# Optimization experiments

Measured on AMD Instinct MI355X. Metric: run time of the kernel, lower is better.

Reference implementation:

```python
import jax, jax.numpy as jnp
import numpy as np

D_MODEL = 2048
NQ = 16      # query heads
NKV = 4      # kv heads (GQA)
DH = 128     # content head dim
DR = 64      # rope head dim
DKV = 512    # kv latent dim
DQC = 1536   # q latent dim
B, S = 2, 2048
DT = DH + DR


def rotate_half(x):
    x1, x2 = jnp.split(x, 2, axis=-1)
    return jnp.concatenate([-x2, x1], axis=-1)


def setup_inputs() -> dict:
    key = jax.random.key(0)
    ks = jax.random.split(key, 10)
    sc = 0.02
    x = jax.random.normal(ks[0], (B, S, D_MODEL), jnp.float32)
    positions = jnp.arange(S, dtype=jnp.int32)
    # standard RoPE cache over the rope subspace
    inv_freq = 1.0 / (10000.0 ** (jnp.arange(0, DR, 2, dtype=jnp.float32) / DR))
    ang = positions.astype(jnp.float32)[:, None] * inv_freq[None, :]   # [S, DR/2]
    emb = jnp.concatenate([ang, ang], axis=-1)                         # [S, DR]
    cos_cache = jnp.cos(emb)
    sin_cache = jnp.sin(emb)
    attn_mask = jnp.tril(jnp.ones((S, S), dtype=bool))                 # causal, True=attend
    # weights stored [in, out] (torch Linear weight transposed)
    W_DKV = sc * jax.random.normal(ks[1], (D_MODEL, DKV), jnp.float32)
    W_UK = sc * jax.random.normal(ks[2], (DKV, NKV * DH), jnp.float32)
    W_UV = sc * jax.random.normal(ks[3], (DKV, NKV * DH), jnp.float32)
    W_DQ = sc * jax.random.normal(ks[4], (D_MODEL, DQC), jnp.float32)
    W_UQ = sc * jax.random.normal(ks[5], (DQC, NQ * DH), jnp.float32)
    W_KR = sc * jax.random.normal(ks[6], (D_MODEL, NKV * DR), jnp.float32)
    W_QR = sc * jax.random.normal(ks[7], (D_MODEL, NQ * DR), jnp.float32)
    W_O = sc * jax.random.normal(ks[8], (NQ * DH, D_MODEL), jnp.float32)
    return {"x": x, "cos_cache": cos_cache, "sin_cache": sin_cache,
            "positions": positions, "attn_mask": attn_mask,
            "W_DKV": W_DKV, "W_UK": W_UK, "W_UV": W_UV, "W_DQ": W_DQ,
            "W_UQ": W_UQ, "W_KR": W_KR, "W_QR": W_QR, "W_O": W_O}


def reference(x, cos_cache, sin_cache, positions, attn_mask,
              W_DKV, W_UK, W_UV, W_DQ, W_UQ, W_KR, W_QR, W_O):
    b, s, _ = x.shape
    cos = cos_cache[positions][None, None]  # [1,1,S,DR]
    sin = sin_cache[positions][None, None]
    # low-rank KV latent (this is the MLA cache)
    c_kv = x @ W_DKV                                                 # [B,S,DKV]
    K_rope = (x @ W_KR).reshape(b, s, NKV, DR).transpose(0, 2, 1, 3)  # [B,NKV,S,DR]
    K_rope = K_rope * cos + rotate_half(K_rope) * sin
    # decompress K/V content from latent
    K_content = (c_kv @ W_UK).reshape(b, s, NKV, DH).transpose(0, 2, 1, 3)  # [B,NKV,S,DH]
    V = (c_kv @ W_UV).reshape(b, s, NKV, DH).transpose(0, 2, 1, 3)          # [B,NKV,S,DH]
    # queries via low-rank path + rope subspace
    c_q = x @ W_DQ
    Q_content = (c_q @ W_UQ).reshape(b, s, NQ, DH).transpose(0, 2, 1, 3)    # [B,NQ,S,DH]
    Q_rope = (x @ W_QR).reshape(b, s, NQ, DR).transpose(0, 2, 1, 3)         # [B,NQ,S,DR]
    Q_rope = Q_rope * cos + rotate_half(Q_rope) * sin
    Q = jnp.concatenate([Q_content, Q_rope], axis=-1)   # [B,NQ,S,DT]
    K = jnp.concatenate([K_content, K_rope], axis=-1)   # [B,NKV,S,DT]
    # GQA: group query heads over shared kv heads (no materialized repeat)
    G = NQ // NKV
    Qg = Q.reshape(b, NKV, G, s, DT)
    scores = jnp.einsum('bkgsd,bktd->bkgst', Qg, K) / np.float32(np.sqrt(DT))
    scores = jnp.where(attn_mask[None, None, None], scores, -jnp.inf)
    w = jax.nn.softmax(scores, axis=-1)
    attn = jnp.einsum('bkgst,bktd->bkgsd', w, V)         # [B,NKV,G,S,DH]
    attn = attn.reshape(b, NQ, s, DH).transpose(0, 2, 1, 3).reshape(b, s, NQ * DH)
    out = attn @ W_O                                     # [B,S,D_MODEL]
    return out, c_kv, K_rope
```

## Files before the change

kernel.cpp:

```cpp
#include <hip/hip_runtime.h>
#include <stdint.h>

typedef unsigned short u16;
typedef unsigned int u32;

#define B_    2
#define S_    2048
#define NQ_   16
#define NKV_  4
#define DH_   128
#define DR_   64
#define DT_   192
#define M_    4096

using short8 = __attribute__((ext_vector_type(8))) short;
using f32x4  = __attribute__((ext_vector_type(4))) float;
using half8  = __attribute__((ext_vector_type(8))) _Float16;
using u16x4  = __attribute__((ext_vector_type(4))) u16;

__device__ __forceinline__ float cl(float f) {
    return fminf(fmaxf(f, -3.38e38f), 3.38e38f);
}
__device__ __forceinline__ u16 f2b(float f) {
    union { float f; u32 u; } v; v.f = f;
    u32 u = v.u;
    return (u16)((u + 0x7fffu + ((u >> 16) & 1u)) >> 16);
}
__device__ __forceinline__ void gload16(const void* g, void* l) {
    __builtin_amdgcn_global_load_lds(
        (const __attribute__((address_space(1))) void*)g,
        (__attribute__((address_space(3))) void*)l,
        16, 0, 0);
}

__device__ __forceinline__ void wt_body(const float* __restrict__ W,
                                        _Float16* __restrict__ T,
                                        int K, int N, int kx, int ny,
                                        float (*tile)[33]) {
    int k0 = kx * 32, n0 = ny * 32;
    int tx = threadIdx.x, ty = threadIdx.y;
#pragma unroll
    for (int i = 0; i < 32; i += 8)
        tile[ty + i][tx] = W[(size_t)(k0 + ty + i) * N + n0 + tx];
    __syncthreads();
#pragma unroll
    for (int i = 0; i < 32; i += 8)
        T[(size_t)(n0 + ty + i) * K + k0 + tx] = (_Float16)tile[tx][ty + i];
}

__global__ __launch_bounds__(256) void prep_all(const float* __restrict__ x,
                                                _Float16* __restrict__ xf,
                                                const float* __restrict__ W_DKV,
                                                const float* __restrict__ W_KR,
                                                const float* __restrict__ W_DQ,
                                                const float* __restrict__ W_QR,
                                                const float* __restrict__ W_UQ,
                                                const float* __restrict__ W_UK,
                                                const float* __restrict__ W_UV,
                                                const float* __restrict__ W_O,
                                                _Float16* __restrict__ Wmeg,
                                                _Float16* __restrict__ Wuq,
                                                _Float16* __restrict__ Wukv,
                                                _Float16* __restrict__ Wo) {
    __shared__ float tile[32][33];
    const int id = blockIdx.x;
    if (id < 1024) {
        wt_body(W_DKV, Wmeg, 2048, 512, id & 63, id >> 6, tile);
    } else if (id < 1536) {
        int l = id - 1024;
        wt_body(W_KR, Wmeg + (size_t)512 * 2048, 2048, 256, l & 63, l >> 6, tile);
    } else if (id < 4608) {
        int l = id - 1536;
        wt_body(W_DQ, Wmeg + (size_t)768 * 2048, 2048, 1536, l & 63, l >> 6, tile);
    } else if (id < 6656) {
        int l = id - 4608;
        wt_body(W_QR, Wmeg + (size_t)2304 * 2048, 2048, 1024, l & 63, l >> 6, tile);
    } else if (id < 9728) {
        int l = id - 6656;
        wt_body(W_UQ, Wuq, 1536, 2048, l % 48, l / 48, tile);
    } else if (id < 9984) {
        int l = id - 9728;
        wt_body(W_UK, Wukv, 512, 512, l & 15, l >> 4, tile);
    } else if (id < 10240) {
        int l = id - 9984;
        wt_body(W_UV, Wukv + (size_t)512 * 512, 512, 512, l & 15, l >> 4, tile);
    } else if (id < 14336) {
        int l = id - 10240;
        wt_body(W_O, Wo, 2048, 2048, l & 63, l >> 6, tile);
    } else {
        int l = id - 14336;
        int t1 = threadIdx.y * 32 + threadIdx.x;
        size_t i = ((size_t)l * 256 + t1) * 8;
        float4 a = *(const float4*)(x + i);
        float4 b4 = *(const float4*)(x + i + 4);
        float va[8] = {a.x, a.y, a.z, a.w, b4.x, b4.y, b4.z, b4.w};
        half8 f;
#pragma unroll
        for (int j = 0; j < 8; ++j) f[j] = (_Float16)va[j];
        *(half8*)(xf + i) = f;
    }
}

__device__ __forceinline__ void gemm_body(const _Float16* __restrict__ A, int lda,
                                          const _Float16* __restrict__ Bt,
                                          void* p0, void* p1,
                                          float cscale, int mode,
                                          int N, int K, int bx,
                                          _Float16* lA, _Float16* lB) {
    const int t = threadIdx.x, lane = t & 63, w = t >> 6;
    const int quad = lane >> 4, l16 = lane & 15;
    const int wr = w >> 1, wc = w & 1;
    const int m0 = blockIdx.y * 128, n0 = bx * 128;
    f32x4 acc[4][4] = {};

    for (int kt = 0; kt < K; kt += 32) {
        __syncthreads();
#pragma unroll
        for (int c = 0; c < 2; ++c) {
            const int chunk = c * 256 + t;
            const int row = chunk >> 2, co = (chunk & 3) * 8;
            const int lofs = (c * 256 + w * 64) * 8;
            gload16(A + (size_t)(m0 + row) * lda + kt + co, lA + lofs);
            gload16(Bt + (size_t)(n0 + row) * K + kt + co, lB + lofs);
        }
        __syncthreads();
        half8 af[4], bf4[4];
#pragma unroll
        for (int i = 0; i < 4; ++i) {
            af[i]  = *(const half8*)&lA[(wr * 64 + i * 16 + l16) * 32 + quad * 8];
            bf4[i] = *(const half8*)&lB[(wc * 64 + i * 16 + l16) * 32 + quad * 8];
        }
#pragma unroll
        for (int i = 0; i < 4; ++i)
#pragma unroll
            for (int j = 0; j < 4; ++j)
                acc[i][j] = __builtin_amdgcn_mfma_f32_16x16x32_f16(af[i], bf4[j], acc[i][j], 0, 0, 0);
    }
#pragma unroll
    for (int i = 0; i < 4; ++i)
#pragma unroll
        for (int j = 0; j < 4; ++j) {
            const int mbase = m0 + wr * 64 + i * 16 + quad * 4;
            const int nn = n0 + wc * 64 + j * 16 + l16;
            if (mode == 3) {
                const int bb = mbase >> 11, s = mbase & 2047;
                if (nn < 512) {
                    u16* Kp = (u16*)p0;
                    const int kv = nn >> 7, d = nn & 127;
                    const size_t rb = ((size_t)((bb * 4 + kv) * 2048 + s)) * 192 + d;
#pragma unroll
                    for (int r = 0; r < 4; ++r)
                        Kp[rb + (size_t)r * 192] = f2b(acc[i][j][r]);
                } else {
                    u16* Vt = (u16*)p1;
                    const int e = nn - 512, kv = e >> 7, d = e & 127;
                    u16x4 pk;
                    pk[0] = f2b(acc[i][j][0]); pk[1] = f2b(acc[i][j][1]);
                    pk[2] = f2b(acc[i][j][2]); pk[3] = f2b(acc[i][j][3]);
                    *(u16x4*)&((u16*)Vt)[((size_t)((bb * 4 + kv) * 128 + d)) * 2048 + s] = pk;
                }
            } else {
                float* C = (float*)p0;
#pragma unroll
                for (int r = 0; r < 4; ++r)
                    C[(size_t)(mbase + r) * N + nn] = cl(acc[i][j][r]);
            }
        }
}

__global__ __launch_bounds__(256) void gemm_f16(const _Float16* __restrict__ A, int lda,
                                                const _Float16* __restrict__ Bt,
                                                void* p0, void* p1,
                                                float cscale, int mode,
                                                int N, int K) {
    __shared__ __align__(16) _Float16 lA[128 * 32];
    __shared__ __align__(16) _Float16 lB[128 * 32];
    gemm_body(A, lda, Bt, p0, p1, cscale, mode, N, K, blockIdx.x, lA, lB);
}

__global__ __launch_bounds__(512) void gemm2ph(const _Float16* __restrict__ A, int lda,
                                               const _Float16* __restrict__ Bt,
                                               void* p0, void* p1, void* p2,
                                               void* p3, void* p4,
                                               float cscale, int mode,
                                               int N, int K, int NBX) {
    __shared__ __align__(16) _Float16 lA[2][128 * 64];
    __shared__ __align__(16) _Float16 lB[2][256 * 64];
    const int t = threadIdx.x, lane = t & 63, w = t >> 6;
    const int quad = lane >> 4, l16 = lane & 15;
    const int wr = w >> 2, wc = w & 3;
    const int id = blockIdx.x;
    const int cpx = (NBX * 32) >> 3;
    const int swz = (id & 7) * cpx + (id >> 3);
    const int bx = swz % NBX, by = swz / NBX;
    const int m0 = by * 128, n0 = bx * 256;
    f32x4 acc[4][4] = {};

    auto STAGE = [&](int buf, int kt) {
#pragma unroll
        for (int q = 0; q < 2; ++q) {
            const int chunk = q * 512 + t;
            const int row = chunk >> 3, cop = chunk & 7;
            const int co = (cop ^ (row & 7)) * 8;
            gload16(A + (size_t)(m0 + row) * lda + kt + co,
                    lA[buf] + (q * 512 + w * 64) * 8);
        }
#pragma unroll
        for (int q = 0; q < 4; ++q) {
            const int chunk = q * 512 + t;
            const int row = chunk >> 3, cop = chunk & 7;
            const int co = (cop ^ (row & 7)) * 8;
            gload16(Bt + (size_t)(n0 + row) * K + kt + co,
                    lB[buf] + (q * 512 + w * 64) * 8);
        }
    };

    STAGE(0, 0);
    __syncthreads();
    int cur = 0;
    for (int kt = 0; kt < K; kt += 64) {
        if (kt + 64 < K) STAGE(cur ^ 1, kt + 64);
        const _Float16* bufA = lA[cur];
        const _Float16* bufB = lB[cur];
#pragma unroll
        for (int kc = 0; kc < 2; ++kc) {
            half8 af[4], bf[4];
#pragma unroll
            for (int i = 0; i < 4; ++i) {
                const int r = wr * 64 + i * 16 + l16;
                af[i] = *(const half8*)&bufA[(r * 8 + ((kc * 4 + quad) ^ (r & 7))) * 8];
            }
#pragma unroll
            for (int j = 0; j < 4; ++j) {
                const int r = wc * 64 + j * 16 + l16;
                bf[j] = *(const half8*)&bufB[(r * 8 + ((kc * 4 + quad) ^ (r & 7))) * 8];
            }
#pragma unroll
            for (int i = 0; i < 4; ++i)
#pragma unroll
                for (int j = 0; j < 4; ++j)
                    acc[i][j] = __builtin_amdgcn_mfma_f32_16x16x32_f16(af[i], bf[j], acc[i][j], 0, 0, 0);
        }
        __syncthreads();
        cur ^= 1;
    }
#pragma unroll
    for (int i = 0; i < 4; ++i)
#pragma unroll
        for (int j = 0; j < 4; ++j) {
            const int mbase = m0 + wr * 64 + i * 16 + quad * 4;
            const int nn = n0 + wc * 64 + j * 16 + l16;
            if (mode == 0) {
                float* C = (float*)p0;
#pragma unroll
                for (int r = 0; r < 4; ++r)
                    C[(size_t)(mbase + r) * N + nn] = cl(acc[i][j][r]);
            } else if (mode == 2) {
                u16* Q = (u16*)p0;
                const int h = nn >> 7, dcol = nn & 127;
#pragma unroll
                for (int r = 0; r < 4; ++r)
                    Q[(size_t)(mbase + r) * 3072 + h * 192 + dcol] =
                        f2b(acc[i][j][r] * cscale);
            } else {
                if (nn < 512) {
                    float* ckv = (float*)p0;
                    _Float16* ckf = (_Float16*)p1;
#pragma unroll
                    for (int r = 0; r < 4; ++r) {
                        float v = acc[i][j][r];
                        ckv[(size_t)(mbase + r) * 512 + nn] = cl(v);
                        ckf[(size_t)(mbase + r) * 512 + nn] = (_Float16)v;
                    }
                } else if (nn < 768) {
                    float* krr = (float*)p2;
#pragma unroll
                    for (int r = 0; r < 4; ++r)
                        krr[(size_t)(mbase + r) * 256 + (nn - 512)] = acc[i][j][r];
                } else if (nn < 2304) {
                    _Float16* dqc = (_Float16*)p3;
#pragma unroll
                    for (int r = 0; r < 4; ++r)
                        dqc[(size_t)(mbase + r) * 1536 + (nn - 768)] = (_Float16)acc[i][j][r];
                } else {
                    _Float16* qrf = (_Float16*)p4;
#pragma unroll
                    for (int r = 0; r < 4; ++r)
                        qrf[(size_t)(mbase + r) * 1024 + (nn - 2304)] = (_Float16)acc[i][j][r];
                }
            }
        }
}

__global__ __launch_bounds__(256) void rope_all(const _Float16* __restrict__ qrf,
                                                const float* __restrict__ krr,
                                                const float* __restrict__ cosc,
                                                const float* __restrict__ sinc,
                                                const int* __restrict__ pos,
                                                u16* __restrict__ qb16,
                                                float* __restrict__ Krope,
                                                u16* __restrict__ Kp) {
    const float sc = 0.07216878364870322f;
    if ((int)blockIdx.x < 8192) {
        int t = blockIdx.x * 256 + threadIdx.x;
        int d = t & 31, h = (t >> 5) & 15, rowi = t >> 9;
        int s = rowi & 2047;
        int p = pos[s];
        float c1 = cosc[p * 64 + d],      s1 = sinc[p * 64 + d];
        float c2 = cosc[p * 64 + 32 + d], s2 = sinc[p * 64 + 32 + d];
        const _Float16* base = qrf + (size_t)rowi * 1024 + h * 64;
        float x1 = (float)base[d];
        float x2 = (float)base[d + 32];
        u16* q = qb16 + (size_t)rowi * 3072 + h * 192 + 128;
        q[d]      = f2b((x1 * c1 - x2 * s1) * sc);
        q[d + 32] = f2b((x2 * c2 + x1 * s2) * sc);
    } else {
        int t = (blockIdx.x - 8192) * 256 + threadIdx.x;
        int d = t & 31, kv = (t >> 5) & 3, rowi = t >> 7;
        int b = rowi >> 11, s = rowi & 2047;
        int p = pos[s];
        float c1 = cosc[p * 64 + d],      s1 = sinc[p * 64 + d];
        float c2 = cosc[p * 64 + 32 + d], s2 = sinc[p * 64 + 32 + d];
        float x1 = krr[(size_t)rowi * 256 + kv * 64 + d];
        float x2 = krr[(size_t)rowi * 256 + kv * 64 + 32 + d];
        float o1 = x1 * c1 - x2 * s1;
        float o2 = x2 * c2 + x1 * s2;
        int g = b * NKV_ + kv;
        size_t ob = ((size_t)(g * S_) + s) * 64;
        Krope[ob + d]      = cl(o1);
        Krope[ob + 32 + d] = cl(o2);
        u16* kp = Kp + ((size_t)(g * S_ + s)) * 192 + 128;
        kp[d]      = f2b(o1);
        kp[32 + d] = f2b(o2);
    }
}

__global__ __launch_bounds__(256) void attn_mfma(const u16* __restrict__ qb16,
                                                 const u16* __restrict__ Kp,
                                                 const u16* __restrict__ Vt,
                                                 _Float16* __restrict__ atf) {
    __shared__ __align__(16) u16 lK[64 * 200];
    __shared__ __align__(16) u16 lVt[144 * 72];
    __shared__ __align__(16) u16 lP[4][16 * 72];

    const int t = threadIdx.x, lane = t & 63, w = t >> 6;
    const int quad = lane >> 4, l16 = lane & 15;
    const int id = blockIdx.x;
    const int g = id & 7;
    const int b = g >> 2;
    const int k = id >> 3;
    const int h = (g & 3) * 4 + (k & 3);
    const int px = k >> 2;

#pragma unroll
    for (int c = 0; c < 4; ++c) {
        int i = c * 256 + t;
        int rr = 128 + (i >> 6), ccol = i & 63;
        lVt[rr * 72 + ccol] = (rr == 128) ? (u16)0x3F80 : (u16)0;
    }

    for (int ph = 0; ph < 2; ++ph) {
        const int qt = ph ? px : (31 - px);
        const int q0 = qt * 64;
        const int iw = q0 + w * 16;

        short8 qf[6];
        {
            const u16* qp = qb16 + ((size_t)(b * S_ + iw + l16)) * 3072 + h * 192;
#pragma unroll
            for (int kc = 0; kc < 6; ++kc)
                qf[kc] = *(const short8*)&qp[kc * 32 + quad * 8];
        }

        f32x4 O9[9] = {};
        float mr[4] = {-1e30f, -1e30f, -1e30f, -1e30f};

        const int ntile = qt + 1;
        for (int tile = 0; tile < ntile; ++tile) {
            const int j0 = tile * 64;
            __syncthreads();
#pragma unroll
            for (int c = 0; c < 6; ++c) {
                int seg = c * 256 + t;
                int row = seg / 24, ch = (seg % 24) * 8;
                *(uint4*)&lK[row * 200 + ch] =
                    *(const uint4*)&Kp[((size_t)g * S_ + j0 + row) * 192 + ch];
            }
#pragma unroll
            for (int c = 0; c < 4; ++c) {
                int seg = c * 256 + t;
                int d = seg >> 3, ch = (seg & 7) * 8;
                *(uint4*)&lVt[d * 72 + ch] =
                    *(const uint4*)&Vt[((size_t)g * 128 + d) * S_ + j0 + ch];
            }
            __syncthreads();

            f32x4 s4[4];
            __builtin_amdgcn_s_setprio(1);
#pragma unroll
            for (int cc = 0; cc < 4; ++cc) {
                f32x4 sx = {};
#pragma unroll
                for (int kc = 0; kc < 6; ++kc) {
                    short8 kf = *(const short8*)&lK[(cc * 16 + l16) * 200 + kc * 32 + quad * 8];
                    sx = __builtin_amdgcn_mfma_f32_16x16x32_bf16(qf[kc], kf, sx, 0, 0, 0);
                }
                s4[cc] = sx;
            }
            __builtin_amdgcn_s_setprio(0);

            float sv[4][4];
#pragma unroll
            for (int cc = 0; cc < 4; ++cc)
#pragma unroll
                for (int r = 0; r < 4; ++r) {
                    int ir = iw + quad * 4 + r;
                    sv[cc][r] = (j0 + cc * 16 + l16 <= ir) ? s4[cc][r] : -1e30f;
                }
            float tm[4];
#pragma unroll
            for (int r = 0; r < 4; ++r)
                tm[r] = fmaxf(fmaxf(sv[0][r], sv[1][r]), fmaxf(sv[2][r], sv[3][r]));
#pragma unroll
            for (int m = 1; m < 16; m <<= 1)
#pragma unroll
                for (int r = 0; r < 4; ++r) tm[r] = fmaxf(tm[r], __shfl_xor(tm[r], m));
            int small = (tm[0] <= mr[0] + 8.f) && (tm[1] <= mr[1] + 8.f) &&
                        (tm[2] <= mr[2] + 8.f) && (tm[3] <= mr[3] + 8.f);
            if (!__all(small)) {
                float al[4];
#pragma unroll
                for (int r = 0; r < 4; ++r) {
                    float mn = fmaxf(mr[r], tm[r]);
                    al[r] = __expf(mr[r] - mn);
                    mr[r] = mn;
                }
#pragma unroll
                for (int dc = 0; dc < 9; ++dc)
#pragma unroll
                    for (int r = 0; r < 4; ++r) O9[dc][r] *= al[r];
            }
            float p[4][4];
#pragma unroll
            for (int cc = 0; cc < 4; ++cc)
#pragma unroll
                for (int r = 0; r < 4; ++r)
                    p[cc][r] = __expf(sv[cc][r] - mr[r]);
#pragma unroll
            for (int cc = 0; cc < 4; ++cc)
#pragma unroll
                for (int r = 0; r < 4; ++r)
                    lP[w][(quad * 4 + r) * 72 + cc * 16 + l16] = f2b(p[cc][r]);
            short8 pf0 = *(const short8*)&lP[w][l16 * 72 + quad * 8];
            short8 pf1 = *(const short8*)&lP[w][l16 * 72 + 32 + quad * 8];
            __builtin_amdgcn_s_setprio(1);
#pragma unroll
            for (int dc = 0; dc < 9; ++dc) {
                short8 vf0 = *(const short8*)&lVt[(dc * 16 + l16) * 72 + quad * 8];
                short8 vf1 = *(const short8*)&lVt[(dc * 16 + l16) * 72 + 32 + quad * 8];
                O9[dc] = __builtin_amdgcn_mfma_f32_16x16x32_bf16(pf0, vf0, O9[dc], 0, 0, 0);
                O9[dc] = __builtin_amdgcn_mfma_f32_16x16x32_bf16(pf1, vf1, O9[dc], 0, 0, 0);
            }
            __builtin_amdgcn_s_setprio(0);
        }
        float inv[4];
#pragma unroll
        for (int r = 0; r < 4; ++r) {
            float lr = __shfl(O9[8][r], quad * 16);
            inv[r] = 1.f / fmaxf(lr, 1e-30f);
        }
#pragma unroll
        for (int dc = 0; dc < 8; ++dc)
#pragma unroll
            for (int r = 0; r < 4; ++r) {
                int ir = iw + quad * 4 + r;
                atf[((size_t)(b * S_ + ir)) * 2048 + h * 128 + dc * 16 + l16] =
                    (_Float16)cl(O9[dc][r] * inv[r]);
            }
    }
}

extern "C" void kernel_launch(void* const* d_in, const int* in_sizes, int n_in,
                              void* d_out, int out_size, void* d_ws, size_t ws_size,
                              hipStream_t stream) {
    const float* x     = (const float*)d_in[0];
    const float* cosc  = (const float*)d_in[1];
    const float* sinc  = (const float*)d_in[2];
    const int*   pos   = (const int*)d_in[3];
    const float* W_DKV = (const float*)d_in[5];
    const float* W_UK  = (const float*)d_in[6];
    const float* W_UV  = (const float*)d_in[7];
    const float* W_DQ  = (const float*)d_in[8];
    const float* W_UQ  = (const float*)d_in[9];
    const float* W_KR  = (const float*)d_in[10];
    const float* W_QR  = (const float*)d_in[11];
    const float* W_O   = (const float*)d_in[12];
    (void)ws_size;

    float* outp      = (float*)d_out;
    float* ckv_out   = outp + 8388608;
    float* krope_out = outp + 10485760;

    char* w = (char*)d_ws;
    auto alloc = [&](size_t bytes) { char* p = w; w += bytes; return p; };
    _Float16* xf   = (_Float16*)alloc(16777216);
    _Float16* ckf  = (_Float16*)alloc(4194304);
    float*    krr  = (float*)alloc(4194304);
    _Float16* dqc  = (_Float16*)alloc(12582912);
    _Float16* qrf  = (_Float16*)alloc(8388608);
    u16*      qb16 = (u16*)alloc(25165824);
    u16*      Kp   = (u16*)alloc(6291456);
    u16*      Vt   = (u16*)alloc(4194304);
    _Float16* atf  = (_Float16*)alloc(16777216);
    _Float16* Wmeg = (_Float16*)alloc(13631488);
    _Float16* Wuq  = (_Float16*)alloc(6291456);
    _Float16* Wukv = (_Float16*)alloc(1048576);
    _Float16* Wo   = (_Float16*)alloc(8388608);

    const float sc = 0.07216878364870322f;

    prep_all<<<18432, dim3(32, 8), 0, stream>>>(x, xf,
                                                W_DKV, W_KR, W_DQ, W_QR,
                                                W_UQ, W_UK, W_UV, W_O,
                                                Wmeg, Wuq, Wukv, Wo);

    gemm2ph<<<416, 512, 0, stream>>>(xf, 2048, Wmeg,
                                     ckv_out, ckf, krr, dqc, qrf,
                                     1.f, 6, 3328, 2048, 13);
    gemm2ph<<<256, 512, 0, stream>>>(dqc, 1536, Wuq,
                                     qb16, nullptr, nullptr, nullptr, nullptr,
                                     sc, 2, 2048, 1536, 8);
    gemm_f16<<<dim3(8, 32), 256, 0, stream>>>(ckf, 512, Wukv,
                                              Kp, Vt, 1.f, 3, 1024, 512);

    rope_all<<<10240, 256, 0, stream>>>(qrf, krr, cosc, sinc, pos,
                                        qb16, krope_out, Kp);

    attn_mfma<<<512, 256, 0, stream>>>(qb16, Kp, Vt, atf);
    gemm2ph<<<256, 512, 0, stream>>>(atf, 2048, Wo,
                                     outp, nullptr, nullptr, nullptr, nullptr,
                                     1.f, 0, 2048, 2048, 8);
}
```

Measured before the change: 437.7 us.

## Merge Q/KV up-projection GEMMs and RoPE into one launch with new K32 GEMM body

Adds a double-buffered GEMM body with BK=32 and XOR-swizzled LDS, used by the first projection GEMM (replacing the BK=64 variant) and by a new combined stage3 kernel. stage3 runs the Q up-projection, the K/V up-projection and the RoPE elementwise work as block ranges of a single launch, cutting three launches to one and letting independent work overlap. The risk is a race: the RoPE blocks write into qb16 and Kp, which the GEMM blocks of the same launch also write (different columns). The RoPE step itself only reads qrf/krr from the earlier kernel, so ordering holds, but the smaller K-tile may reduce GEMM efficiency.

```diff
diff --git a/kernel.cpp b/kernel.cpp
--- a/kernel.cpp
+++ b/kernel.cpp
@@ -101,40 +101,62 @@
     }
 }
 
-__device__ __forceinline__ void gemm_body(const _Float16* __restrict__ A, int lda,
-                                          const _Float16* __restrict__ Bt,
-                                          void* p0, void* p1,
-                                          float cscale, int mode,
-                                          int N, int K, int bx,
-                                          _Float16* lA, _Float16* lB) {
+__device__ __forceinline__ void g2ph32_body(const _Float16* __restrict__ A, int lda,
+                                            const _Float16* __restrict__ Bt,
+                                            void* p0, void* p1, void* p2,
+                                            void* p3, void* p4,
+                                            float cscale, int mode,
+                                            int N, int K, int NBX, int id,
+                                            _Float16 (*lA)[128 * 32],
+                                            _Float16 (*lB)[256 * 32]) {
     const int t = threadIdx.x, lane = t & 63, w = t >> 6;
     const int quad = lane >> 4, l16 = lane & 15;
-    const int wr = w >> 1, wc = w & 1;
-    const int m0 = blockIdx.y * 128, n0 = bx * 128;
+    const int wr = w >> 2, wc = w & 3;
+    const int cpx = (NBX * 32) >> 3;
+    const int swz = (id & 7) * cpx + (id >> 3);
+    const int bx = swz % NBX, by = swz / NBX;
+    const int m0 = by * 128, n0 = bx * 256;
     f32x4 acc[4][4] = {};
 
+    auto STAGE = [&](int buf, int kt) {
+        {
+            const int chunk = t;
+            const int row = chunk >> 2, cop = chunk & 3;
+            const int co = (cop ^ ((row >> 1) & 3)) * 8;
+            gload16(A + (size_t)(m0 + row) * lda + kt + co, lA[buf] + chunk * 8);
+        }
+#pragma unroll
+        for (int q = 0; q < 2; ++q) {
+            const int chunk = q * 512 + t;
+            const int row = chunk >> 2, cop = chunk & 3;
+            const int co = (cop ^ ((row >> 1) & 3)) * 8;
+            gload16(Bt + (size_t)(n0 + row) * K + kt + co, lB[buf] + chunk * 8);
+        }
+    };
+
+    STAGE(0, 0);
+    __syncthreads();
+    int cur = 0;
     for (int kt = 0; kt < K; kt += 32) {
+        if (kt + 32 < K) STAGE(cur ^ 1, kt + 32);
+        half8 af[4], bf[4];
+#pragma unroll
+        for (int i = 0; i < 4; ++i) {
+            const int r = wr * 64 + i * 16 + l16;
+            af[i] = *(const half8*)&lA[cur][(r * 4 + (quad ^ ((r >> 1) & 3))) * 8];
+        }
+#pragma unroll
+        for (int j = 0; j < 4; ++j) {
+            const int r = wc * 64 + j * 16 + l16;
+            bf[j] = *(const half8*)&lB[cur][(r * 4 + (quad ^ ((r >> 1) & 3))) * 8];
+        }
+#pragma unroll
+        for (int i = 0; i < 4; ++i)
+#pragma unroll
+            for (int j = 0; j < 4; ++j)
+                acc[i][j] = __builtin_amdgcn_mfma_f32_16x16x32_f16(af[i], bf[j], acc[i][j], 0, 0, 0);
         __syncthreads();
-#pragma unroll
-        for (int c = 0; c < 2; ++c) {
-            const int chunk = c * 256 + t;
-            const int row = chunk >> 2, co = (chunk & 3) * 8;
-            const int lofs = (c * 256 + w * 64) * 8;
-            gload16(A + (size_t)(m0 + row) * lda + kt + co, lA + lofs);
-            gload16(Bt + (size_t)(n0 + row) * K + kt + co, lB + lofs);
-        }
-        __syncthreads();
-        half8 af[4], bf4[4];
-#pragma unroll
-        for (int i = 0; i < 4; ++i) {
-            af[i]  = *(const half8*)&lA[(wr * 64 + i * 16 + l16) * 32 + quad * 8];
-            bf4[i] = *(const half8*)&lB[(wc * 64 + i * 16 + l16) * 32 + quad * 8];
-        }
-#pragma unroll
-        for (int i = 0; i < 4; ++i)
-#pragma unroll
-            for (int j = 0; j < 4; ++j)
-                acc[i][j] = __builtin_amdgcn_mfma_f32_16x16x32_f16(af[i], bf4[j], acc[i][j], 0, 0, 0);
+        cur ^= 1;
     }
 #pragma unroll
     for (int i = 0; i < 4; ++i)
@@ -142,7 +164,19 @@
         for (int j = 0; j < 4; ++j) {
             const int mbase = m0 + wr * 64 + i * 16 + quad * 4;
             const int nn = n0 + wc * 64 + j * 16 + l16;
-            if (mode == 3) {
+            if (mode == 0) {
+                float* C = (float*)p0;
+#pragma unroll
+                for (int r = 0; r < 4; ++r)
+                    C[(size_t)(mbase + r) * N + nn] = cl(acc[i][j][r]);
+            } else if (mode == 2) {
+                u16* Q = (u16*)p0;
+                const int h = nn >> 7, dcol = nn & 127;
+#pragma unroll
+                for (int r = 0; r < 4; ++r)
+                    Q[(size_t)(mbase + r) * 3072 + h * 192 + dcol] =
+                        f2b(acc[i][j][r] * cscale);
+            } else if (mode == 3) {
                 const int bb = mbase >> 11, s = mbase & 2047;
                 if (nn < 512) {
                     u16* Kp = (u16*)p0;
@@ -160,28 +194,110 @@
                     *(u16x4*)&((u16*)Vt)[((size_t)((bb * 4 + kv) * 128 + d)) * 2048 + s] = pk;
                 }
             } else {
-                float* C = (float*)p0;
-#pragma unroll
-                for (int r = 0; r < 4; ++r)
-                    C[(size_t)(mbase + r) * N + nn] = cl(acc[i][j][r]);
-            }
-        }
-}
-
-__global__ __launch_bounds__(256) void gemm_f16(const _Float16* __restrict__ A, int lda,
-                                                const _Float16* __restrict__ Bt,
-                                                void* p0, void* p1,
-                                                float cscale, int mode,
-                                                int N, int K) {
-    __shared__ __align__(16) _Float16 lA[128 * 32];
-    __shared__ __align__(16) _Float16 lB[128 * 32];
-    gemm_body(A, lda, Bt, p0, p1, cscale, mode, N, K, blockIdx.x, lA, lB);
+                if (nn < 512) {
+                    float* ckv = (float*)p0;
+                    _Float16* ckf = (_Float16*)p1;
+#pragma unroll
+                    for (int r = 0; r < 4; ++r) {
+                        float v = acc[i][j][r];
+                        ckv[(size_t)(mbase + r) * 512 + nn] = cl(v);
+                        ckf[(size_t)(mbase + r) * 512 + nn] = (_Float16)v;
+                    }
+                } else if (nn < 768) {
+                    float* krr = (float*)p2;
+#pragma unroll
+                    for (int r = 0; r < 4; ++r)
+                        krr[(size_t)(mbase + r) * 256 + (nn - 512)] = acc[i][j][r];
+                } else if (nn < 2304) {
+                    _Float16* dqc = (_Float16*)p3;
+#pragma unroll
+                    for (int r = 0; r < 4; ++r)
+                        dqc[(size_t)(mbase + r) * 1536 + (nn - 768)] = (_Float16)acc[i][j][r];
+                } else {
+                    _Float16* qrf = (_Float16*)p4;
+#pragma unroll
+                    for (int r = 0; r < 4; ++r)
+                        qrf[(size_t)(mbase + r) * 1024 + (nn - 2304)] = (_Float16)acc[i][j][r];
+                }
+            }
+        }
+}
+
+__global__ __launch_bounds__(512) void gemm_mega(const _Float16* __restrict__ xf,
+                                                 const _Float16* __restrict__ Wmeg,
+                                                 float* __restrict__ ckv,
+                                                 _Float16* __restrict__ ckf,
+                                                 float* __restrict__ krr,
+                                                 _Float16* __restrict__ dqc,
+                                                 _Float16* __restrict__ qrf) {
+    __shared__ __align__(16) _Float16 lA[2][128 * 32];
+    __shared__ __align__(16) _Float16 lB[2][256 * 32];
+    g2ph32_body(xf, 2048, Wmeg, ckv, ckf, krr, dqc, qrf,
+                1.f, 6, 3328, 2048, 13, blockIdx.x, lA, lB);
+}
+
+__global__ __launch_bounds__(512) void stage3(const _Float16* __restrict__ dqc,
+                                              const _Float16* __restrict__ Wuq,
+                                              u16* __restrict__ qb16, float scq,
+                                              const _Float16* __restrict__ ckf,
+                                              const _Float16* __restrict__ Wukv,
+                                              u16* __restrict__ Kp,
+                                              u16* __restrict__ Vt,
+                                              const _Float16* __restrict__ qrf,
+                                              const float* __restrict__ krr,
+                                              const float* __restrict__ cosc,
+                                              const float* __restrict__ sinc,
+                                              const int* __restrict__ pos,
+                                              float* __restrict__ Krope) {
+    __shared__ __align__(16) _Float16 lA[2][128 * 32];
+    __shared__ __align__(16) _Float16 lB[2][256 * 32];
+    const int id = blockIdx.x;
+    if (id < 256) {
+        g2ph32_body(dqc, 1536, Wuq, qb16, nullptr, nullptr, nullptr, nullptr,
+                    scq, 2, 2048, 1536, 8, id, lA, lB);
+    } else if (id < 384) {
+        g2ph32_body(ckf, 512, Wukv, Kp, Vt, nullptr, nullptr, nullptr,
+                    1.f, 3, 1024, 512, 4, id - 256, lA, lB);
+    } else {
+        const float sc = 0.07216878364870322f;
+        int ti = (id - 384) * 512 + threadIdx.x;
+        if (ti < 4096 * 16 * 32) {
+            int d = ti & 31, h = (ti >> 5) & 15, rowi = ti >> 9;
+            int s = rowi & 2047;
+            int p = pos[s];
+            float c1 = cosc[p * 64 + d],      s1 = sinc[p * 64 + d];
+            float c2 = cosc[p * 64 + 32 + d], s2 = sinc[p * 64 + 32 + d];
+            const _Float16* base = qrf + (size_t)rowi * 1024 + h * 64;
+            float x1 = (float)base[d];
+            float x2 = (float)base[d + 32];
+            u16* q = qb16 + (size_t)rowi * 3072 + h * 192 + 128;
+            q[d]      = f2b((x1 * c1 - x2 * s1) * sc);
+            q[d + 32] = f2b((x2 * c2 + x1 * s2) * sc);
+        } else {
+            int t2 = ti - 4096 * 16 * 32;
+            int d = t2 & 31, kv = (t2 >> 5) & 3, rowi = t2 >> 7;
+            int b = rowi >> 11, s = rowi & 2047;
+            int p = pos[s];
+            float c1 = cosc[p * 64 + d],      s1 = sinc[p * 64 + d];
+            float c2 = cosc[p * 64 + 32 + d], s2 = sinc[p * 64 + 32 + d];
+            float x1 = krr[(size_t)rowi * 256 + kv * 64 + d];
+            float x2 = krr[(size_t)rowi * 256 + kv * 64 + 32 + d];
+            float o1 = x1 * c1 - x2 * s1;
+            float o2 = x2 * c2 + x1 * s2;
+            int g = b * NKV_ + kv;
+            size_t ob = ((size_t)(g * S_) + s) * 64;
+            Krope[ob + d]      = cl(o1);
+            Krope[ob + 32 + d] = cl(o2);
+            u16* kp = Kp + ((size_t)(g * S_ + s)) * 192 + 128;
+            kp[d]      = f2b(o1);
+            kp[32 + d] = f2b(o2);
+        }
+    }
 }
 
 __global__ __launch_bounds__(512) void gemm2ph(const _Float16* __restrict__ A, int lda,
                                                const _Float16* __restrict__ Bt,
-                                               void* p0, void* p1, void* p2,
-                                               void* p3, void* p4,
+                                               void* p0,
                                                float cscale, int mode,
                                                int N, int K, int NBX) {
     __shared__ __align__(16) _Float16 lA[2][128 * 64];
@@ -250,89 +366,12 @@
         for (int j = 0; j < 4; ++j) {
             const int mbase = m0 + wr * 64 + i * 16 + quad * 4;
             const int nn = n0 + wc * 64 + j * 16 + l16;
-            if (mode == 0) {
-                float* C = (float*)p0;
-#pragma unroll
-                for (int r = 0; r < 4; ++r)
-                    C[(size_t)(mbase + r) * N + nn] = cl(acc[i][j][r]);
-            } else if (mode == 2) {
-                u16* Q = (u16*)p0;
-                const int h = nn >> 7, dcol = nn & 127;
-#pragma unroll
-                for (int r = 0; r < 4; ++r)
-                    Q[(size_t)(mbase + r) * 3072 + h * 192 + dcol] =
-                        f2b(acc[i][j][r] * cscale);
-            } else {
-                if (nn < 512) {
-                    float* ckv = (float*)p0;
-                    _Float16* ckf = (_Float16*)p1;
-#pragma unroll
-                    for (int r = 0; r < 4; ++r) {
-                        float v = acc[i][j][r];
-                        ckv[(size_t)(mbase + r) * 512 + nn] = cl(v);
-                        ckf[(size_t)(mbase + r) * 512 + nn] = (_Float16)v;
-                    }
-                } else if (nn < 768) {
-                    float* krr = (float*)p2;
-#pragma unroll
-                    for (int r = 0; r < 4; ++r)
-                        krr[(size_t)(mbase + r) * 256 + (nn - 512)] = acc[i][j][r];
-                } else if (nn < 2304) {
-                    _Float16* dqc = (_Float16*)p3;
-#pragma unroll
-                    for (int r = 0; r < 4; ++r)
-                        dqc[(size_t)(mbase + r) * 1536 + (nn - 768)] = (_Float16)acc[i][j][r];
-                } else {
-                    _Float16* qrf = (_Float16*)p4;
-#pragma unroll
-                    for (int r = 0; r < 4; ++r)
-                        qrf[(size_t)(mbase + r) * 1024 + (nn - 2304)] = (_Float16)acc[i][j][r];
-                }
-            }
-        }
-}
-
-__global__ __launch_bounds__(256) void rope_all(const _Float16* __restrict__ qrf,
-                                                const float* __restrict__ krr,
-                                                const float* __restrict__ cosc,
-                                                const float* __restrict__ sinc,
-                                                const int* __restrict__ pos,
-                                                u16* __restrict__ qb16,
-                                                float* __restrict__ Krope,
-                                                u16* __restrict__ Kp) {
-    const float sc = 0.07216878364870322f;
-    if ((int)blockIdx.x < 8192) {
-        int t = blockIdx.x * 256 + threadIdx.x;
-        int d = t & 31, h = (t >> 5) & 15, rowi = t >> 9;
-        int s = rowi & 2047;
-        int p = pos[s];
-        float c1 = cosc[p * 64 + d],      s1 = sinc[p * 64 + d];
-        float c2 = cosc[p * 64 + 32 + d], s2 = sinc[p * 64 + 32 + d];
-        const _Float16* base = qrf + (size_t)rowi * 1024 + h * 64;
-        float x1 = (float)base[d];
-        float x2 = (float)base[d + 32];
-        u16* q = qb16 + (size_t)rowi * 3072 + h * 192 + 128;
-        q[d]      = f2b((x1 * c1 - x2 * s1) * sc);
-        q[d + 32] = f2b((x2 * c2 + x1 * s2) * sc);
-    } else {
-        int t = (blockIdx.x - 8192) * 256 + threadIdx.x;
-        int d = t & 31, kv = (t >> 5) & 3, rowi = t >> 7;
-        int b = rowi >> 11, s = rowi & 2047;
-        int p = pos[s];
-        float c1 = cosc[p * 64 + d],      s1 = sinc[p * 64 + d];
-        float c2 = cosc[p * 64 + 32 + d], s2 = sinc[p * 64 + 32 + d];
-        float x1 = krr[(size_t)rowi * 256 + kv * 64 + d];
-        float x2 = krr[(size_t)rowi * 256 + kv * 64 + 32 + d];
-        float o1 = x1 * c1 - x2 * s1;
-        float o2 = x2 * c2 + x1 * s2;
-        int g = b * NKV_ + kv;
-        size_t ob = ((size_t)(g * S_) + s) * 64;
-        Krope[ob + d]      = cl(o1);
-        Krope[ob + 32 + d] = cl(o2);
-        u16* kp = Kp + ((size_t)(g * S_ + s)) * 192 + 128;
-        kp[d]      = f2b(o1);
-        kp[32 + d] = f2b(o2);
-    }
+            float* C = (float*)p0;
+#pragma unroll
+            for (int r = 0; r < 4; ++r)
+                C[(size_t)(mbase + r) * N + nn] = cl(acc[i][j][r]);
+        }
+    (void)cscale; (void)mode;
 }
 
 __global__ __launch_bounds__(256) void attn_mfma(const u16* __restrict__ qb16,
@@ -524,20 +563,13 @@
                                                 W_UQ, W_UK, W_UV, W_O,
                                                 Wmeg, Wuq, Wukv, Wo);
 
-    gemm2ph<<<416, 512, 0, stream>>>(xf, 2048, Wmeg,
-                                     ckv_out, ckf, krr, dqc, qrf,
-                                     1.f, 6, 3328, 2048, 13);
-    gemm2ph<<<256, 512, 0, stream>>>(dqc, 1536, Wuq,
-                                     qb16, nullptr, nullptr, nullptr, nullptr,
-                                     sc, 2, 2048, 1536, 8);
-    gemm_f16<<<dim3(8, 32), 256, 0, stream>>>(ckf, 512, Wukv,
-                                              Kp, Vt, 1.f, 3, 1024, 512);
-
-    rope_all<<<10240, 256, 0, stream>>>(qrf, krr, cosc, sinc, pos,
-                                        qb16, krope_out, Kp);
+    gemm_mega<<<416, 512, 0, stream>>>(xf, Wmeg, ckv_out, ckf, krr, dqc, qrf);
+
+    stage3<<<5504, 512, 0, stream>>>(dqc, Wuq, qb16, sc,
+                                     ckf, Wukv, Kp, Vt,
+                                     qrf, krr, cosc, sinc, pos, krope_out);
 
     attn_mfma<<<512, 256, 0, stream>>>(qb16, Kp, Vt, atf);
     gemm2ph<<<256, 512, 0, stream>>>(atf, 2048, Wo,
-                                     outp, nullptr, nullptr, nullptr, nullptr,
-                                     1.f, 0, 2048, 2048, 8);
-}
+                                     outp, 1.f, 0, 2048, 2048, 8);
+}
```

After: 435.1 us. About the same (-0.6%).
